# Kernel optimization log

Measured on AMD Instinct MI355X. Metric: run time of the kernel, lower is better.

Reference implementation:

```python
import jax, jax.numpy as jnp
import numpy as np

B, L, D = 4, 4096, 1024


def hippo_freqs(dim):
    n = np.arange(dim, dtype=np.float32)
    f = np.sqrt(2 * n + 1)
    f = f / f.max()
    return np.exp(-f * np.log(10000)).astype(np.float32)


def setup_inputs() -> dict:
    key = jax.random.key(0)
    ks = jax.random.split(key, 8)
    s = 1.0 / np.sqrt(D)
    return {
        "x": jax.random.normal(ks[0], (B, L, D), dtype=jnp.float32),
        "omega": jnp.asarray(hippo_freqs(D)),
        "log_gamma": jax.random.normal(ks[1], (D,), dtype=jnp.float32) - 3.0,
        "dt": jnp.float32(0.1),
        "W_psi": jax.random.uniform(ks[2], (2 * D, D), jnp.float32, -s, s),
        "b_psi": jax.random.uniform(ks[3], (2 * D,), jnp.float32, -s, s),
        "W_phi": jax.random.uniform(ks[4], (2 * D, D), jnp.float32, -s, s),
        "b_phi": jax.random.uniform(ks[5], (2 * D,), jnp.float32, -s, s),
        "W_gate": jax.random.uniform(ks[6], (D, D), jnp.float32, -s, s),
        "b_gate": jax.random.uniform(ks[7], (D,), jnp.float32, -s, s),
    }


def _proj(z):
    # exact_projection: per-channel-axis standardization over last dim (biased var)
    mean = z.mean(axis=-1, keepdims=True)
    var = ((z - mean) ** 2).mean(axis=-1, keepdims=True)
    return (z - mean) / (jnp.sqrt(var) + 1e-6)


def reference(x, omega, log_gamma, dt, W_psi, b_psi, W_phi, b_phi, W_gate, b_gate):
    Bn, Ln, Dn = x.shape
    psi_raw = jnp.einsum("bld,ed->ble", x, W_psi) + b_psi
    phi_raw = jnp.einsum("bld,ed->ble", x, W_phi) + b_phi
    psi = jax.lax.complex(psi_raw[..., :Dn], psi_raw[..., Dn:])
    phi = jax.lax.complex(phi_raw[..., :Dn], phi_raw[..., Dn:])
    gate = jax.nn.sigmoid(jnp.einsum("bld,ed->ble", x, W_gate) + b_gate)
    U = gate.astype(psi.dtype) * psi  # [B,L,D] complex

    dt_abs = jnp.abs(dt)
    lam = jax.lax.complex(-jnp.exp(log_gamma), omega)  # [D]
    t_axis = jnp.arange(Ln, dtype=jnp.float32)
    kernel = jnp.exp(lam[None, :] * t_axis[:, None].astype(lam.dtype) * dt_abs)  # [L,D]

    n_fft = 2 * Ln
    Kf = jnp.fft.fft(kernel, n=n_fft, axis=0)          # [2L,D]
    Uf = jnp.fft.fft(U, n=n_fft, axis=1)               # [B,2L,D]
    H = jnp.fft.ifft(Uf * Kf[None], axis=1)[:, :Ln]    # causal conv, [B,L,D]

    H_proj = jax.lax.complex(_proj(H.real), _proj(H.imag))
    return (H_proj * jnp.conj(phi)).real
```

## Files before the change

### kernel.cpp

```cpp
#include <hip/hip_runtime.h>
#include <hip/hip_bf16.h>
#include <math.h>

#define B_ 4
#define L_ 4096
#define D_ 1024
#define M_ (B_*L_)
#define N_ 5120
#define K_ 1024
#define CHUNKS 128
#define LC 32
#define PL ((long)M_ * D_)

#define WS_NEEDED 211812352ull

typedef __attribute__((ext_vector_type(8))) short bf16x8;
typedef __attribute__((ext_vector_type(4))) float f32x4;
typedef __attribute__((ext_vector_type(4))) unsigned short u16x4;

__device__ inline float b2f(short s) {
    unsigned u = ((unsigned)(unsigned short)s) << 16;
    float f; __builtin_memcpy(&f, &u, 4); return f;
}
__device__ inline unsigned short f2bu(float f) {
    __hip_bfloat16 h = __float2bfloat16(f);
    unsigned short u; __builtin_memcpy(&u, &h, 2); return u;
}

__device__ inline void cvt4(const float4* __restrict__ src, ushort* __restrict__ dst, long j) {
    float4 v = src[j];
    __hip_bfloat16 a = __float2bfloat16(v.x), b = __float2bfloat16(v.y),
                   c = __float2bfloat16(v.z), d = __float2bfloat16(v.w);
    ushort4 o = { *(ushort*)&a, *(ushort*)&b, *(ushort*)&c, *(ushort*)&d };
    *(ushort4*)(dst + j * 4) = o;
}

__global__ void convert_kernel(const float* __restrict__ x,
                               const float* __restrict__ Wpsi,
                               const float* __restrict__ Wphi,
                               const float* __restrict__ Wgate,
                               ushort* __restrict__ xb,
                               ushort* __restrict__ wb) {
    long i0 = (long)blockIdx.x * blockDim.x + threadIdx.x;
    long stride = (long)gridDim.x * blockDim.x;
    const long nx4 = ((long)M_ * K_) >> 2;
    for (long j = i0; j < nx4; j += stride) cvt4((const float4*)x, xb, j);
    const long nW14 = (2048L * 1024) >> 2, nW34 = (1024L * 1024) >> 2;
    for (long j = i0; j < nW14; j += stride) cvt4((const float4*)Wpsi, wb, j);
    for (long j = i0; j < nW14; j += stride) cvt4((const float4*)Wphi, wb + 2048L * 1024, j);
    for (long j = i0; j < nW34; j += stride) cvt4((const float4*)Wgate, wb + 4096L * 1024, j);
}

#define BM2 256
#define BN2 256
#define BK2 64
#define NT  (K_ / BK2)
#define DBUF_BYTES 65536

#define STAGE(gptr, brow, kt, slotoff)                                                       \
  do {                                                                                       \
    const __hip_bfloat16* g0_ = (gptr) + (long)((brow) + srow0) * K_ + (kt) * 64 + sgc0 * 8; \
    const __hip_bfloat16* g1_ = (gptr) + (long)((brow) + srow1) * K_ + (kt) * 64 + sgc1 * 8; \
    __builtin_amdgcn_global_load_lds((const __attribute__((address_space(1))) void*)g0_,     \
        (__attribute__((address_space(3))) void*)(smem + (slotoff) + ldst0), 16, 0, 0);      \
    __builtin_amdgcn_global_load_lds((const __attribute__((address_space(1))) void*)g1_,     \
        (__attribute__((address_space(3))) void*)(smem + (slotoff) + ldst1), 16, 0, 0);      \
  } while (0)

#define RDA1(db, qm, i_)                                                            \
  do {                                                                              \
    aA[i_][0] = *(const bf16x8*)((db) + aoff + (qm) * 8192 + (i_) * 2048 + ct0);    \
    aA[i_][1] = *(const bf16x8*)((db) + aoff + (qm) * 8192 + (i_) * 2048 + ct1);    \
  } while (0)
#define RDB1(db, qn, s, j_)                                                         \
  do {                                                                              \
    bB[s][j_][0] = *(const bf16x8*)((db) + boff + (qn) * 4096 + (j_) * 2048 + ct0); \
    bB[s][j_][1] = *(const bf16x8*)((db) + boff + (qn) * 4096 + (j_) * 2048 + ct1); \
  } while (0)

#define MFMA16(qm, qn, s)                                                                         \
  _Pragma("unroll") for (int i_ = 0; i_ < 4; ++i_)                                                \
    _Pragma("unroll") for (int j_ = 0; j_ < 2; ++j_) {                                            \
      acc[(qm)*4+i_][(qn)*2+j_] = __builtin_amdgcn_mfma_f32_16x16x32_bf16(                        \
          aA[i_][0], bB[s][j_][0], acc[(qm)*4+i_][(qn)*2+j_], 0, 0, 0);                           \
      acc[(qm)*4+i_][(qn)*2+j_] = __builtin_amdgcn_mfma_f32_16x16x32_bf16(                        \
          aA[i_][1], bB[s][j_][1], acc[(qm)*4+i_][(qn)*2+j_], 0, 0, 0);                           \
    }
#define BARRIER __builtin_amdgcn_s_barrier()

#define COMPUTE_TILE(db)                                                                          \
  do {                                                                                            \
    RDA1(db, 0, 0); RDB1(db, 0, 0, 0); RDB1(db, 0, 0, 1);                                         \
    RDA1(db, 0, 1); RDA1(db, 0, 2); RDA1(db, 0, 3);                                               \
    __builtin_amdgcn_s_setprio(1); MFMA16(0, 0, 0); __builtin_amdgcn_s_setprio(0);                \
    RDB1(db, 1, 1, 0); RDB1(db, 1, 1, 1);                                                         \
    __builtin_amdgcn_s_setprio(1); MFMA16(0, 1, 1); __builtin_amdgcn_s_setprio(0);                \
    RDA1(db, 1, 0); RDA1(db, 1, 1); RDA1(db, 1, 2); RDA1(db, 1, 3);                               \
    __builtin_amdgcn_s_setprio(1); MFMA16(1, 1, 1); MFMA16(1, 0, 0);                              \
    __builtin_amdgcn_s_setprio(0);                                                                \
  } while (0)

__global__ __launch_bounds__(512, 2)
void gemm_kernel(const __hip_bfloat16* __restrict__ xb,
                 const __hip_bfloat16* __restrict__ wb,
                 const float* __restrict__ b_psi,
                 const float* __restrict__ b_phi,
                 const float* __restrict__ b_gate,
                 __hip_bfloat16* __restrict__ raw5) {
    __shared__ __attribute__((aligned(16))) char smem[2 * DBUF_BYTES];

    const int tid   = threadIdx.x;
    const int wid   = tid >> 6;
    const int lane  = tid & 63;
    const int row16 = lane & 15;
    const int quad  = lane >> 4;
    const int wm    = wid >> 2;
    const int wn    = wid & 3;

    const int bid = blockIdx.y * 64 + blockIdx.x;
    const int swz = (bid & 7) * (1280 / 8) + (bid >> 3);
    const int m_blk = (swz & 63) * BM2;
    const int n_blk = (swz >> 6) * BN2;

    const int srow0 = tid >> 3;
    const int srow1 = (512 + tid) >> 3;
    const int sch   = tid & 7;
    const int sgc0  = sch ^ (srow0 & 7);
    const int sgc1  = sch ^ (srow1 & 7);
    const int ldst0 = (wid * 64) * 16;
    const int ldst1 = (512 + wid * 64) * 16;

    const int sw   = row16 & 7;
    const int aoff = wm * 16384 + row16 * 128;
    const int boff = 32768 + (wn >> 1) * 16384 + ((wn & 1) * 64 + row16) * 128;
    const int ct0  = ((0 * 4 + quad) ^ sw) * 16;
    const int ct1  = ((1 * 4 + quad) ^ sw) * 16;

    bf16x8 aA[4][2];
    bf16x8 bB[2][2][2];
    f32x4  acc[8][4] = {};

    STAGE(xb, m_blk,       0, 0);
    STAGE(xb, m_blk + 128, 0, 16384);
    STAGE(wb, n_blk,       0, 32768);
    STAGE(wb, n_blk + 128, 0, 32768 + 16384);
    asm volatile("s_waitcnt vmcnt(0)" ::: "memory");
    BARRIER;

    for (int t = 0; t < NT - 1; ++t) {
        char* db = smem + (t & 1) * DBUF_BYTES;
        const int nb = ((t + 1) & 1) * DBUF_BYTES;
        STAGE(xb, m_blk,       t + 1, nb);
        STAGE(xb, m_blk + 128, t + 1, nb + 16384);
        STAGE(wb, n_blk,       t + 1, nb + 32768);
        STAGE(wb, n_blk + 128, t + 1, nb + 32768 + 16384);
        COMPUTE_TILE(db);
        asm volatile("s_waitcnt vmcnt(0)" ::: "memory");
        BARRIER;
    }
    {
        char* db = smem + ((NT - 1) & 1) * DBUF_BYTES;
        COMPUTE_TILE(db);
    }

#pragma unroll
    for (int mi = 0; mi < 8; ++mi) {
        const int mbase = m_blk + wm * 128 + (mi >> 2) * 64 + (mi & 3) * 16 + quad * 4;
#pragma unroll
        for (int nj = 0; nj < 4; ++nj) {
            int n = n_blk + wn * 64 + (nj >> 1) * 32 + (nj & 1) * 16 + row16;
            float bias = (n < 2048) ? b_psi[n] : (n < 4096) ? b_phi[n - 2048] : b_gate[n - 4096];
            int g = n >> 10, d = n & 1023;
            __hip_bfloat16* pl = raw5 + (long)g * PL;
#pragma unroll
            for (int r = 0; r < 4; ++r)
                pl[(long)(mbase + r) * D_ + d] = __float2bfloat16(acc[mi][nj][r] + bias);
        }
    }
}

__global__ __launch_bounds__(256) void scan1_kernel(__hip_bfloat16* raw5,
                                                    const float* __restrict__ omega,
                                                    const float* __restrict__ log_gamma,
                                                    const float* __restrict__ dtp,
                                                    float2* __restrict__ E) {
    const int d0 = threadIdx.x * 4;
    const int c  = blockIdx.x;
    const int b  = blockIdx.y;
    const float dt = fabsf(dtp[0]);

    float ar[4], ai[4];
#pragma unroll
    for (int q = 0; q < 4; ++q) {
        float decay = expf(-expf(log_gamma[d0 + q]) * dt);
        float ang = omega[d0 + q] * dt;
        ar[q] = decay * cosf(ang);
        ai[q] = decay * sinf(ang);
    }

    ushort* Pre = (ushort*)raw5;
    ushort* Pim = (ushort*)(raw5 + PL);
    const ushort* Gt = (const ushort*)(raw5 + 4 * PL);
    long base = (long)(b * L_ + c * LC) * D_ + d0;

    float hr[4] = {0.f, 0.f, 0.f, 0.f}, hi[4] = {0.f, 0.f, 0.f, 0.f};
    for (int i = 0; i < LC; i++) {
        long idx = base + (long)i * D_;
        u16x4 pr = *(const u16x4*)(Pre + idx);
        u16x4 pi = *(const u16x4*)(Pim + idx);
        u16x4 gt = *(const u16x4*)(Gt + idx);
        u16x4 orr, oii;
#pragma unroll
        for (int q = 0; q < 4; ++q) {
            float sg = 1.f / (1.f + expf(-b2f((short)gt[q])));
            float ur = sg * b2f((short)pr[q]);
            float ui = sg * b2f((short)pi[q]);
            float nr = ar[q] * hr[q] - ai[q] * hi[q] + ur;
            float ni = ar[q] * hi[q] + ai[q] * hr[q] + ui;
            hr[q] = nr; hi[q] = ni;
            orr[q] = f2bu(nr);
            oii[q] = f2bu(ni);
        }
        *(u16x4*)(Pre + idx) = orr;
        *(u16x4*)(Pim + idx) = oii;
    }
    float2* Eo = E + ((long)c * B_ + b) * D_ + d0;
#pragma unroll
    for (int q = 0; q < 4; ++q) Eo[q] = make_float2(hr[q], hi[q]);
}

__global__ void apow_kernel(const float* __restrict__ omega,
                            const float* __restrict__ log_gamma,
                            const float* __restrict__ dtp,
                            float2* __restrict__ apow) {
    int t = blockIdx.x * blockDim.x + threadIdx.x;
    int i = t >> 10, d = t & 1023;
    float dt = fabsf(dtp[0]);
    float e = expf(-expf(log_gamma[d]) * dt * (float)(i + 1));
    float ang = omega[d] * dt * (float)(i + 1);
    apow[t] = make_float2(e * cosf(ang), e * sinf(ang));
}

__global__ __launch_bounds__(128) void carry_kernel(const float2* __restrict__ E,
                                                    const float* __restrict__ omega,
                                                    const float* __restrict__ log_gamma,
                                                    const float* __restrict__ dtp,
                                                    float2* __restrict__ carry) {
    __shared__ float2 sh[CHUNKS];
    const int c = threadIdx.x;
    const int bd = blockIdx.x;
    const int b = bd >> 10, d = bd & 1023;
    const float dt = fabsf(dtp[0]);
    const float gd = expf(log_gamma[d]);
    const float wd = omega[d];

    float2 v = E[((long)c * B_ + b) * D_ + d];
    sh[c] = v;
    __syncthreads();
#pragma unroll
    for (int s = 1; s < CHUNKS; s <<= 1) {
        float2 prev;
        bool has = (c >= s);
        if (has) prev = sh[c - s];
        __syncthreads();
        if (has) {
            float t = dt * (float)LC * (float)s;
            float dec = expf(-gd * t);
            float ang = wd * t;
            float Ar = dec * cosf(ang), Ai = dec * sinf(ang);
            v.x += Ar * prev.x - Ai * prev.y;
            v.y += Ar * prev.y + Ai * prev.x;
            sh[c] = v;
        }
        __syncthreads();
    }
    float2 outv = (c == 0) ? make_float2(0.f, 0.f) : sh[c - 1];
    carry[((long)c * B_ + b) * D_ + d] = outv;
}

__global__ __launch_bounds__(256) void finish_kernel(const __hip_bfloat16* __restrict__ raw5,
                                                     const float2* __restrict__ carry,
                                                     const float2* __restrict__ apow,
                                                     float* __restrict__ out) {
    const int wv = threadIdx.x >> 6, lane = threadIdx.x & 63;
    const int r = blockIdx.x * 4 + wv;
    const int l = r & (L_ - 1);
    const int b = r >> 12;
    const int c = l >> 5, i = l & 31;
    const int d0 = lane * 16;
    const long base = (long)r * D_ + d0;

    const __hip_bfloat16* Hre = raw5;
    const __hip_bfloat16* Him = raw5 + PL;
    const __hip_bfloat16* Pre = raw5 + 2 * PL;
    const __hip_bfloat16* Pim = raw5 + 3 * PL;
    const float2* cr = carry + ((long)c * B_ + b) * D_ + d0;
    const float2* ap = apow + (long)i * D_ + d0;

    bf16x8 hre[2], him[2];
    hre[0] = *(const bf16x8*)(Hre + base);     hre[1] = *(const bf16x8*)(Hre + base + 8);
    him[0] = *(const bf16x8*)(Him + base);     him[1] = *(const bf16x8*)(Him + base + 8);

    float hr[16], hi[16];
    float s0 = 0.f, s1 = 0.f, s2 = 0.f, s3 = 0.f;
#pragma unroll
    for (int j = 0; j < 16; j++) {
        float2 cv = cr[j];
        float2 av = ap[j];
        float fr = av.x * cv.x - av.y * cv.y;
        float fi = av.x * cv.y + av.y * cv.x;
        float xr = b2f(hre[j >> 3][j & 7]) + fr;
        float xi = b2f(him[j >> 3][j & 7]) + fi;
        hr[j] = xr; hi[j] = xi;
        s0 += xr; s1 += xr * xr; s2 += xi; s3 += xi * xi;
    }
#pragma unroll
    for (int m = 1; m < 64; m <<= 1) {
        s0 += __shfl_xor(s0, m);
        s1 += __shfl_xor(s1, m);
        s2 += __shfl_xor(s2, m);
        s3 += __shfl_xor(s3, m);
    }
    float mean_r = s0 * (1.f / D_);
    float var_r  = s1 * (1.f / D_) - mean_r * mean_r;
    float mean_i = s2 * (1.f / D_);
    float var_i  = s3 * (1.f / D_) - mean_i * mean_i;
    float inv_r = 1.f / (sqrtf(fmaxf(var_r, 0.f)) + 1e-6f);
    float inv_i = 1.f / (sqrtf(fmaxf(var_i, 0.f)) + 1e-6f);

    bf16x8 pre[2], pim[2];
    pre[0] = *(const bf16x8*)(Pre + base);     pre[1] = *(const bf16x8*)(Pre + base + 8);
    pim[0] = *(const bf16x8*)(Pim + base);     pim[1] = *(const bf16x8*)(Pim + base + 8);

    float o[16];
#pragma unroll
    for (int j = 0; j < 16; j++)
        o[j] = (hr[j] - mean_r) * inv_r * b2f(pre[j >> 3][j & 7])
             + (hi[j] - mean_i) * inv_i * b2f(pim[j >> 3][j & 7]);
#pragma unroll
    for (int q = 0; q < 4; q++)
        *(float4*)(out + base + q * 4) = make_float4(o[q*4], o[q*4+1], o[q*4+2], o[q*4+3]);
}

extern "C" void kernel_launch(void* const* d_in, const int* in_sizes, int n_in,
                              void* d_out, int out_size, void* d_ws, size_t ws_size,
                              hipStream_t stream) {
    (void)in_sizes; (void)n_in; (void)out_size;
    if (ws_size < WS_NEEDED) return;

    const float* x         = (const float*)d_in[0];
    const float* omega     = (const float*)d_in[1];
    const float* log_gamma = (const float*)d_in[2];
    const float* dt        = (const float*)d_in[3];
    const float* W_psi     = (const float*)d_in[4];
    const float* b_psi     = (const float*)d_in[5];
    const float* W_phi     = (const float*)d_in[6];
    const float* b_phi     = (const float*)d_in[7];
    const float* W_gate    = (const float*)d_in[8];
    const float* b_gate    = (const float*)d_in[9];

    char* ws = (char*)d_ws;
    __hip_bfloat16* xb   = (__hip_bfloat16*)(ws);
    __hip_bfloat16* wb   = (__hip_bfloat16*)(ws + 33554432);
    __hip_bfloat16* raw5 = (__hip_bfloat16*)(ws + 44040192);
    float2* E     = (float2*)(ws);
    float2* carry = (float2*)(ws + 4194304);
    float2* apow  = (float2*)(ws + 8388608);
    float* out = (float*)d_out;

    convert_kernel<<<2048, 256, 0, stream>>>(x, W_psi, W_phi, W_gate, (ushort*)xb, (ushort*)wb);
    gemm_kernel<<<dim3(M_ / BM2, N_ / BN2), 512, 0, stream>>>(xb, wb, b_psi, b_phi, b_gate, raw5);
    apow_kernel<<<128, 256, 0, stream>>>(omega, log_gamma, dt, apow);
    scan1_kernel<<<dim3(CHUNKS, B_), 256, 0, stream>>>(raw5, omega, log_gamma, dt, E);
    carry_kernel<<<B_ * D_, 128, 0, stream>>>(E, omega, log_gamma, dt, carry);
    finish_kernel<<<M_ / 4, 256, 0, stream>>>(raw5, carry, apow, out);
}
```

Before: 445.8 us.

## Halve scan chunk length and replace carry tree scan with sequential per-channel scan

Scan chunks shrink from 32 to 16 steps and double in count to 256, so the local scan runs twice as many blocks with half the serial length. The carry pass now gives each thread one (batch, channel) pair and walks the chunks sequentially, replacing the shared-memory Hillis-Steele scan with its many barriers and per-step exp/sin/cos. scan1 reads the precomputed single-step power from apow instead of recomputing transcendentals. The trade-off is a 256-step serial dependency per thread in the carry kernel and a larger E/carry footprint, which required shifting workspace offsets.

```diff
diff --git a/kernel.cpp b/kernel.cpp
--- a/kernel.cpp
+++ b/kernel.cpp
@@ -8,8 +8,8 @@
 #define M_ (B_*L_)
 #define N_ 5120
 #define K_ 1024
-#define CHUNKS 128
-#define LC 32
+#define CHUNKS 256
+#define LC 16
 #define PL ((long)M_ * D_)
 
 #define WS_NEEDED 211812352ull
@@ -180,22 +180,17 @@
 }
 
 __global__ __launch_bounds__(256) void scan1_kernel(__hip_bfloat16* raw5,
-                                                    const float* __restrict__ omega,
-                                                    const float* __restrict__ log_gamma,
-                                                    const float* __restrict__ dtp,
+                                                    const float2* __restrict__ apow,
                                                     float2* __restrict__ E) {
     const int d0 = threadIdx.x * 4;
     const int c  = blockIdx.x;
     const int b  = blockIdx.y;
-    const float dt = fabsf(dtp[0]);
 
     float ar[4], ai[4];
 #pragma unroll
     for (int q = 0; q < 4; ++q) {
-        float decay = expf(-expf(log_gamma[d0 + q]) * dt);
-        float ang = omega[d0 + q] * dt;
-        ar[q] = decay * cosf(ang);
-        ai[q] = decay * sinf(ang);
+        float2 a = apow[d0 + q];
+        ar[q] = a.x; ai[q] = a.y;
     }
 
     ushort* Pre = (ushort*)raw5;
@@ -241,41 +236,29 @@
     apow[t] = make_float2(e * cosf(ang), e * sinf(ang));
 }
 
-__global__ __launch_bounds__(128) void carry_kernel(const float2* __restrict__ E,
+__global__ __launch_bounds__(256) void carry_kernel(const float2* __restrict__ E,
                                                     const float* __restrict__ omega,
                                                     const float* __restrict__ log_gamma,
                                                     const float* __restrict__ dtp,
                                                     float2* __restrict__ carry) {
-    __shared__ float2 sh[CHUNKS];
-    const int c = threadIdx.x;
-    const int bd = blockIdx.x;
-    const int b = bd >> 10, d = bd & 1023;
+    const int g = blockIdx.x * 256 + threadIdx.x;
+    const int b = g >> 10, d = g & 1023;
     const float dt = fabsf(dtp[0]);
-    const float gd = expf(log_gamma[d]);
-    const float wd = omega[d];
-
-    float2 v = E[((long)c * B_ + b) * D_ + d];
-    sh[c] = v;
-    __syncthreads();
-#pragma unroll
-    for (int s = 1; s < CHUNKS; s <<= 1) {
-        float2 prev;
-        bool has = (c >= s);
-        if (has) prev = sh[c - s];
-        __syncthreads();
-        if (has) {
-            float t = dt * (float)LC * (float)s;
-            float dec = expf(-gd * t);
-            float ang = wd * t;
-            float Ar = dec * cosf(ang), Ai = dec * sinf(ang);
-            v.x += Ar * prev.x - Ai * prev.y;
-            v.y += Ar * prev.y + Ai * prev.x;
-            sh[c] = v;
-        }
-        __syncthreads();
-    }
-    float2 outv = (c == 0) ? make_float2(0.f, 0.f) : sh[c - 1];
-    carry[((long)c * B_ + b) * D_ + d] = outv;
+    const float T = dt * (float)LC;
+    const float dec = expf(-expf(log_gamma[d]) * T);
+    const float ang = omega[d] * T;
+    const float Ar = dec * cosf(ang), Ai = dec * sinf(ang);
+
+    float tr = 0.f, ti = 0.f;
+#pragma unroll 4
+    for (int c = 0; c < CHUNKS; ++c) {
+        const long idx = ((long)c * B_ + b) * D_ + d;
+        carry[idx] = make_float2(tr, ti);
+        float2 e = E[idx];
+        float nr = e.x + Ar * tr - Ai * ti;
+        float ni = e.y + Ar * ti + Ai * tr;
+        tr = nr; ti = ni;
+    }
 }
 
 __global__ __launch_bounds__(256) void finish_kernel(const __hip_bfloat16* __restrict__ raw5,
@@ -286,7 +269,7 @@
     const int r = blockIdx.x * 4 + wv;
     const int l = r & (L_ - 1);
     const int b = r >> 12;
-    const int c = l >> 5, i = l & 31;
+    const int c = l >> 4, i = l & (LC - 1);
     const int d0 = lane * 16;
     const long base = (long)r * D_ + d0;
 
@@ -364,14 +347,14 @@
     __hip_bfloat16* wb   = (__hip_bfloat16*)(ws + 33554432);
     __hip_bfloat16* raw5 = (__hip_bfloat16*)(ws + 44040192);
     float2* E     = (float2*)(ws);
-    float2* carry = (float2*)(ws + 4194304);
-    float2* apow  = (float2*)(ws + 8388608);
+    float2* carry = (float2*)(ws + 8388608);
+    float2* apow  = (float2*)(ws + 16777216);
     float* out = (float*)d_out;
 
     convert_kernel<<<2048, 256, 0, stream>>>(x, W_psi, W_phi, W_gate, (ushort*)xb, (ushort*)wb);
     gemm_kernel<<<dim3(M_ / BM2, N_ / BN2), 512, 0, stream>>>(xb, wb, b_psi, b_phi, b_gate, raw5);
-    apow_kernel<<<128, 256, 0, stream>>>(omega, log_gamma, dt, apow);
-    scan1_kernel<<<dim3(CHUNKS, B_), 256, 0, stream>>>(raw5, omega, log_gamma, dt, E);
-    carry_kernel<<<B_ * D_, 128, 0, stream>>>(E, omega, log_gamma, dt, carry);
+    apow_kernel<<<(LC * D_) / 256, 256, 0, stream>>>(omega, log_gamma, dt, apow);
+    scan1_kernel<<<dim3(CHUNKS, B_), 256, 0, stream>>>(raw5, apow, E);
+    carry_kernel<<<(B_ * D_) / 256, 256, 0, stream>>>(E, omega, log_gamma, dt, carry);
     finish_kernel<<<M_ / 4, 256, 0, stream>>>(raw5, carry, apow, out);
 }
```

Result: no change. 447.7 us (+0.4%).
